# Performance work log

Hardware: AMD Instinct MI355X
Metric: run time of the kernel (lower is better)

## Reference

```python
import jax, jax.numpy as jnp
import numpy as np

NMS_KS = 15
TOP_K = 2048
GAUSS_KS = 7
GAUSS_SIGMA = 1.0
LOSS_LAMBDA = 1.0


def setup_inputs() -> dict:
    key = jax.random.key(0)
    k1, k2, k3 = jax.random.split(key, 3)
    B, H, W = 16, 1024, 1024
    score1 = jax.random.uniform(k1, (B, 1, H, W), dtype=jnp.float32)
    w_score2 = jax.random.uniform(k2, (B, 1, H, W), dtype=jnp.float32)
    w_vis_mask2 = jax.random.randint(k3, (B, 1, H, W), 0, 2) > 0
    return {"score1": score1, "w_score2": w_score2, "w_vis_mask2": w_vis_mask2}


def _nms(score, ks):
    # keep only local maxima within a ks x ks window (stride 1, 'same' padding)
    pooled = jax.lax.reduce_window(score, -jnp.inf, jax.lax.max,
                                   (1, 1, ks, ks), (1, 1, 1, 1), 'SAME')
    return jnp.where(score == pooled, score, jnp.zeros_like(score))


def _prepare_gt_score(score, nms_ks, k, mask):
    # NMS -> mask -> per-image top-k -> binary GT keypoint map
    s = _nms(score, nms_ks) * mask.astype(score.dtype)
    b = s.shape[0]
    flat = s.reshape(b, -1)                      # B x (H*W)
    _, idx = jax.lax.top_k(flat, k)              # B x k
    gt = jnp.zeros_like(flat).at[jnp.arange(b)[:, None], idx].set(1.0)
    return gt.reshape(s.shape)


def _gaussian_filter(x, ks, sigma):
    coords = jnp.arange(ks, dtype=jnp.float32) - (ks - 1) / 2.0
    g = jnp.exp(-(coords ** 2) / (2.0 * sigma ** 2))
    g = g / g.sum()
    k2d = jnp.outer(g, g)[None, None]
    pad = ks // 2
    return jax.lax.conv_general_dilated(
        x, k2d, (1, 1), [(pad, pad), (pad, pad)],
        dimension_numbers=('NCHW', 'OIHW', 'NCHW'))


def reference(score1, w_score2, w_vis_mask2):
    b = score1.shape[0]
    gt_score1 = jax.lax.stop_gradient(
        _prepare_gt_score(w_score2, NMS_KS, TOP_K, w_vis_mask2))
    gt_score1 = _gaussian_filter(gt_score1, GAUSS_KS, GAUSS_SIGMA)
    m = w_vis_mask2.astype(jnp.float32)
    loss = ((score1 - gt_score1) ** 2) * m       # masked elementwise MSE
    loss = loss.reshape(b, -1).sum(-1) / jnp.clip(m.reshape(b, -1).sum(-1), 1e-8)
    return LOSS_LAMBDA * loss.mean()
```

## Files before the change

kernel.cpp:

```cpp
#include <hip/hip_runtime.h>
#include <math.h>

#define BATCH 16
#define H 1024
#define W 1024
#define HR 46
#define CGW 20
#define CGP 21
#define NTILES 8192
#define CAP 4096
#define TOPK 2048
#define BCAP 40

struct WS {
  double term1[BATCH];
  double corr[BATCH];
  unsigned int masksum[BATCH];
  int cand_count[BATCH];
  int   tile_cnt[NTILES];
  float pt1[NTILES * 4];
  int   pmc[NTILES * 4];
  float tile_val[NTILES * BCAP];
  int   tile_idx[NTILES * BCAP];
  float ccand_val[BATCH * CAP];
  int   ccand_idx[BATCH * CAP];
};

__constant__ float GW[7] = {
  0.004433048175f, 0.054005582623f, 0.242036229376f, 0.399050279652f,
  0.242036229376f, 0.054005582623f, 0.004433048175f
};

__device__ __forceinline__ float4 max4(float4 a, float4 b) {
  float4 r;
  r.x = fmaxf(a.x, b.x); r.y = fmaxf(a.y, b.y);
  r.z = fmaxf(a.z, b.z); r.w = fmaxf(a.w, b.w);
  return r;
}

__global__ __launch_bounds__(256, 6) void k_nms(const float* __restrict__ score1,
                                                const float* __restrict__ score2,
                                                const int* __restrict__ mask,
                                                WS* __restrict__ ws) {
  __shared__ float4 halo[HR][CGP];
  __shared__ float4 rmax[32][CGP];
  __shared__ float s_cv[BCAP];
  __shared__ int   s_ci[BCAP];
  __shared__ int   s_cnt;
  const int tid = threadIdx.x;

  const int t = (blockIdx.x & 7) * (NTILES / 8) + (blockIdx.x >> 3);
  const int b  = t >> 9;
  const int tt = t & 511;
  const int ty0 = (tt >> 4) << 5;
  const int tx0 = (tt & 15) << 6;
  const size_t ibase = (size_t)b * ((size_t)H * W);

  if (tid == 0) s_cnt = 0;

  float4 st[4];
  int hr_[4], hc_[4];
  const bool interior = (ty0 >= 7) && (ty0 + 38 < H) && (tx0 >= 8) && (tx0 + 71 < W);
  if (interior) {
    #pragma unroll
    for (int k = 0; k < 4; k++) {
      int i = tid + (k << 8);
      if (i < HR * CGW) {
        int r = i / CGW, c = i - r * CGW;
        hr_[k] = r; hc_[k] = c;
        st[k] = *((const float4*)(score2 + ibase + (size_t)(ty0 - 7 + r) * W + (tx0 - 8)) + c);
      }
    }
  } else {
    #pragma unroll
    for (int k = 0; k < 4; k++) {
      int i = tid + (k << 8);
      if (i < HR * CGW) {
        int r = i / CGW, c = i - r * CGW;
        hr_[k] = r; hc_[k] = c;
        int gy = ty0 - 7 + r, gx = tx0 - 8 + (c << 2);
        float vv[4] = {-INFINITY, -INFINITY, -INFINITY, -INFINITY};
        if (gy >= 0 && gy < H) {
          const float* rp = score2 + ibase + (size_t)gy * W;
          #pragma unroll
          for (int u = 0; u < 4; u++) {
            int gxu = gx + u;
            if (gxu >= 0 && gxu < W) vv[u] = rp[gxu];
          }
        }
        st[k] = make_float4(vv[0], vv[1], vv[2], vv[3]);
      }
    }
  }
  const int prow = tid >> 3;
  const int c8   = tid & 7;
  const size_t pb = ibase + (size_t)(ty0 + prow) * W + tx0 + (c8 << 3);
  const float4 s1a = *(const float4*)(score1 + pb);
  const float4 s1b = *(const float4*)(score1 + pb + 4);
  const int4  mka = *(const int4*)(mask + pb);
  const int4  mkb = *(const int4*)(mask + pb + 4);

  #pragma unroll
  for (int k = 0; k < 4; k++) {
    int i = tid + (k << 8);
    if (i < HR * CGW) halo[hr_[k]][hc_[k]] = st[k];
  }
  __syncthreads();

  if (tid < 160) {
    const int rr = tid / 20;
    const int cg = tid - rr * 20;
    const int R0 = rr << 2;
    float4 core = halo[R0 + 3][cg];
    #pragma unroll
    for (int k = 4; k <= 14; k++) core = max4(core, halo[R0 + k][cg]);
    const float4 h0 = halo[R0][cg], h1 = halo[R0 + 1][cg], h2 = halo[R0 + 2][cg];
    const float4 h15 = halo[R0 + 15][cg], h16 = halo[R0 + 16][cg], h17 = halo[R0 + 17][cg];
    const float4 p2 = h2, p1 = max4(h1, p2), p0 = max4(h0, p1);
    const float4 sf15 = h15, sf16 = max4(sf15, h16), sf17 = max4(sf16, h17);
    rmax[R0 + 0][cg] = max4(core, p0);
    rmax[R0 + 1][cg] = max4(max4(core, p1), sf15);
    rmax[R0 + 2][cg] = max4(max4(core, p2), sf16);
    rmax[R0 + 3][cg] = max4(core, sf17);
  }

  float t1 = 0.f; int mcnt = 0; unsigned int mbits = 0;
  {
    const float sc[8] = {s1a.x, s1a.y, s1a.z, s1a.w, s1b.x, s1b.y, s1b.z, s1b.w};
    const int   mm[8] = {mka.x, mka.y, mka.z, mka.w, mkb.x, mkb.y, mkb.z, mkb.w};
    #pragma unroll
    for (int j = 0; j < 8; j++) {
      if (mm[j]) { t1 = fmaf(sc[j], sc[j], t1); mcnt++; mbits |= (1u << j); }
    }
  }
  __syncthreads();

  float r[24];
  #pragma unroll
  for (int g = 0; g < 6; g++) {
    float4 v = rmax[prow][(c8 << 1) + g];
    r[4 * g + 0] = v.x; r[4 * g + 1] = v.y; r[4 * g + 2] = v.z; r[4 * g + 3] = v.w;
  }
  float core = r[8];
  #pragma unroll
  for (int k = 9; k <= 15; k++) core = fmaxf(core, r[k]);
  const float q7 = r[7];
  const float q6 = fmaxf(r[6], q7);
  const float q5 = fmaxf(r[5], q6);
  const float q4 = fmaxf(r[4], q5);
  const float q3 = fmaxf(r[3], q4);
  const float q2 = fmaxf(r[2], q3);
  const float q1 = fmaxf(r[1], q2);
  float sa[7];
  sa[0] = r[16];
  #pragma unroll
  for (int k = 1; k < 7; k++) sa[k] = fmaxf(sa[k - 1], r[16 + k]);
  float pooled[8];
  pooled[0] = fmaxf(core, q1);
  pooled[1] = fmaxf(fmaxf(core, q2), sa[0]);
  pooled[2] = fmaxf(fmaxf(core, q3), sa[1]);
  pooled[3] = fmaxf(fmaxf(core, q4), sa[2]);
  pooled[4] = fmaxf(fmaxf(core, q5), sa[3]);
  pooled[5] = fmaxf(fmaxf(core, q6), sa[4]);
  pooled[6] = fmaxf(fmaxf(core, q7), sa[5]);
  pooled[7] = fmaxf(core, sa[6]);

  const float4 cva = halo[prow + 7][(c8 << 1) + 2];
  const float4 cvb = halo[prow + 7][(c8 << 1) + 3];
  const float cc[8] = {cva.x, cva.y, cva.z, cva.w, cvb.x, cvb.y, cvb.z, cvb.w};
  #pragma unroll
  for (int j = 0; j < 8; j++) {
    if ((mbits >> j) & 1u) {
      const float s = cc[j];
      if (s == pooled[j] && s > 0.f) {
        int slot = atomicAdd(&s_cnt, 1);
        if (slot < BCAP) {
          s_cv[slot] = s;
          s_ci[slot] = (ty0 + prow) * W + tx0 + (c8 << 3) + j;
        }
      }
    }
  }
  #pragma unroll
  for (int off = 32; off > 0; off >>= 1) {
    t1 += __shfl_down(t1, off);
    mcnt += __shfl_down(mcnt, off);
  }
  if ((tid & 63) == 0) {
    ws->pt1[t * 4 + (tid >> 6)] = t1;
    ws->pmc[t * 4 + (tid >> 6)] = mcnt;
  }
  __syncthreads();
  int cnt = s_cnt; if (cnt > BCAP) cnt = BCAP;
  if (tid == 0) ws->tile_cnt[t] = cnt;
  if (tid < cnt) {
    ws->tile_val[t * BCAP + tid] = s_cv[tid];
    ws->tile_idx[t * BCAP + tid] = s_ci[tid];
  }
}

__global__ __launch_bounds__(256) void k_compact(WS* __restrict__ ws) {
  const int b = blockIdx.x;
  const int tid = threadIdx.x;
  const int lane = tid & 63, w = tid >> 6;
  __shared__ double sF[4];
  __shared__ int    sI[4];
  __shared__ int    wt[4];

  double tsum = 0.0; int msum = 0;
  for (int j = tid; j < 2048; j += 256) {
    tsum += (double)ws->pt1[b * 2048 + j];
    msum += ws->pmc[b * 2048 + j];
  }
  #pragma unroll
  for (int off = 32; off > 0; off >>= 1) {
    tsum += __shfl_down(tsum, off);
    msum += __shfl_down(msum, off);
  }
  if (lane == 0) { sF[w] = tsum; sI[w] = msum; }

  const int tg = b * 512 + 2 * tid;
  int c0 = ws->tile_cnt[tg];     if (c0 > BCAP) c0 = BCAP;
  int c1 = ws->tile_cnt[tg + 1]; if (c1 > BCAP) c1 = BCAP;
  const int pairs = c0 + c1;
  int v = pairs;
  #pragma unroll
  for (int off = 1; off < 64; off <<= 1) {
    int u = __shfl_up(v, off);
    if (lane >= off) v += u;
  }
  if (lane == 63) wt[w] = v;
  __syncthreads();
  if (tid == 0) {
    ws->term1[b] = (sF[0] + sF[1]) + (sF[2] + sF[3]);
    ws->masksum[b] = (unsigned int)(sI[0] + sI[1] + sI[2] + sI[3]);
    ws->corr[b] = 0.0;
  }
  int wo = 0;
  #pragma unroll
  for (int k = 0; k < 4; k++) if (k < w) wo += wt[k];
  const int excl = v - pairs + wo;
  float* dv = ws->ccand_val + b * CAP;
  int*   di = ws->ccand_idx + b * CAP;
  if (tid == 255) {
    int tot = excl + pairs;
    if (tot > CAP) tot = CAP;
    ws->cand_count[b] = tot;
    #pragma unroll
    for (int u = 0; u < 3; u++)
      if (tot + u < CAP) dv[tot + u] = 0.f;
  }
  const float* sv0 = ws->tile_val + (size_t)tg * BCAP;
  const int*   si0 = ws->tile_idx + (size_t)tg * BCAP;
  for (int j = 0; j < c0; j++) {
    int o = excl + j;
    if (o < CAP) { dv[o] = sv0[j]; di[o] = si0[j]; }
  }
  for (int j = 0; j < c1; j++) {
    int o = excl + c0 + j;
    if (o < CAP) { dv[o] = sv0[BCAP + j]; di[o] = si0[BCAP + j]; }
  }
}

__global__ __launch_bounds__(256, 4) void k_rankstamp(const float* __restrict__ score1,
                                                      const int* __restrict__ mask,
                                                      WS* __restrict__ ws) {
  const int blk = (blockIdx.x & 7) * 128 + (blockIdx.x >> 3);
  const int b = blk >> 6;
  const int slice = blk & 63;
  int n = ws->cand_count[b]; if (n > CAP) n = CAP;
  const int i0 = slice << 6;
  if (i0 >= n) return;
  __shared__ __align__(16) float sval[CAP];
  __shared__ __align__(16) int   sidx[CAP];
  __shared__ int   s_prank[4][64];
  __shared__ int   s_keys[64];
  __shared__ int   s_nk;
  __shared__ float cred[4];
  const int tid = threadIdx.x;
  const int nf4 = (n + 3) >> 2;

  const float4* gv = (const float4*)(ws->ccand_val + b * CAP);
  const int4*   gi = (const int4*)(ws->ccand_idx + b * CAP);
  for (int j = tid; j < nf4; j += 256) {
    ((float4*)sval)[j] = gv[j];
    ((int4*)sidx)[j]   = gi[j];
  }
  __syncthreads();

  const int w = tid >> 6, l = tid & 63;
  const float vi = sval[i0 + l];
  const int   xi = sidx[i0 + l];
  const int q = (nf4 + 3) >> 2;
  int lo = w * q; if (lo > nf4) lo = nf4;
  int hi = lo + q; if (hi > nf4) hi = nf4;
  int rank = 0;
  int j = lo;
  for (; j + 4 <= hi; j += 4) {
    #pragma unroll
    for (int u = 0; u < 4; u++) {
      const float4 v = ((const float4*)sval)[j + u];
      const int4  iv = ((const int4*)sidx)[j + u];
      rank += (v.x > vi) + (v.y > vi) + (v.z > vi) + (v.w > vi);
      rank += (v.x == vi && iv.x < xi);
      rank += (v.y == vi && iv.y < xi);
      rank += (v.z == vi && iv.z < xi);
      rank += (v.w == vi && iv.w < xi);
    }
  }
  for (; j < hi; j++) {
    const float4 v = ((const float4*)sval)[j];
    const int4  iv = ((const int4*)sidx)[j];
    rank += (v.x > vi) + (v.y > vi) + (v.z > vi) + (v.w > vi);
    rank += (v.x == vi && iv.x < xi);
    rank += (v.y == vi && iv.y < xi);
    rank += (v.z == vi && iv.z < xi);
    rank += (v.w == vi && iv.w < xi);
  }
  s_prank[w][l] = rank;
  __syncthreads();

  if (tid < 64) {
    const int rtot = s_prank[0][tid] + s_prank[1][tid] + s_prank[2][tid] + s_prank[3][tid];
    const bool sel = (i0 + tid < n) && (rtot < TOPK);
    const unsigned long long bal = __ballot(sel);
    if (sel) {
      const int pos = __popcll(bal & ((1ull << tid) - 1ull));
      s_keys[pos] = sidx[i0 + tid];
    }
    if (tid == 0) s_nk = (int)__popcll(bal);
  }
  __syncthreads();
  const int nk = s_nk;

  float contrib = 0.f;
  const int sub = tid & 7;
  const size_t ib2 = (size_t)b * ((size_t)H * W);
  #pragma unroll
  for (int rnd = 0; rnd < 2; rnd++) {
    const int k = (tid >> 3) + (rnd << 5);
    if (k < nk && sub < 7) {
      const int ck = s_keys[k];
      const int cy = ck >> 10, cx = ck & 1023;
      const int py = cy + sub - 3;
      const float wy = GW[sub] * ((py >= 0 && py < H) ? 1.f : 0.f);
      const int pyc = min(max(py, 0), H - 1);
      const float* s1r = score1 + ib2 + (size_t)pyc * W;
      const int*   mr  = mask   + ib2 + (size_t)pyc * W;
      #pragma unroll
      for (int dx = -3; dx <= 3; dx++) {
        const int px = cx + dx;
        const float wv = wy * GW[dx + 3] * ((px >= 0 && px < W) ? 1.f : 0.f);
        const int pxc = min(max(px, 0), W - 1);
        const float mf = (mr[pxc] != 0) ? 1.f : 0.f;
        contrib += mf * wv * (wv - 2.f * s1r[pxc]);
      }
    }
  }
  #pragma unroll
  for (int off = 32; off > 0; off >>= 1) contrib += __shfl_down(contrib, off);
  if ((tid & 63) == 0) cred[tid >> 6] = contrib;
  __syncthreads();
  if (tid == 0)
    atomicAdd(&ws->corr[b], (double)((cred[0] + cred[1]) + (cred[2] + cred[3])));
}

__global__ void k_final(WS* __restrict__ ws, float* __restrict__ out) {
  const int t = threadIdx.x;
  double v = 0.0;
  if (t < BATCH) {
    double denom = (double)ws->masksum[t];
    if (denom < 1e-8) denom = 1e-8;
    v = (ws->term1[t] + ws->corr[t]) / denom;
  }
  #pragma unroll
  for (int off = 32; off > 0; off >>= 1) v += __shfl_down(v, off);
  if (t == 0) out[0] = (float)(v / BATCH);
}

extern "C" void kernel_launch(void* const* d_in, const int* in_sizes, int n_in,
                              void* d_out, int out_size, void* d_ws, size_t ws_size,
                              hipStream_t stream) {
  const float* score1 = (const float*)d_in[0];
  const float* score2 = (const float*)d_in[1];
  const int*   mask   = (const int*)d_in[2];
  float* out = (float*)d_out;
  WS* ws = (WS*)d_ws;

  k_nms<<<NTILES, 256, 0, stream>>>(score1, score2, mask, ws);
  k_compact<<<BATCH, 256, 0, stream>>>(ws);
  k_rankstamp<<<BATCH * 64, 256, 0, stream>>>(score1, mask, ws);
  k_final<<<1, 64, 0, stream>>>(ws, out);
}
```

Baseline: 82.26 us.

## Make NMS row-max per-wave and emit candidates via wave ballot per band

Each wave now computes the row maxima for its own eight rows, so the second block-wide barrier is replaced by a wave barrier plus an LDS wait. Candidate collection switches from a shared-memory atomic counter plus a final block barrier to a per-wave ballot and popcount, written straight to per-band global slots. Each 8-pixel thread group now keeps at most one local maximum, which holds because the 15x15 window allows at most one maximum per 8 columns. Compaction now scans 8 bands per thread instead of 2 tiles. The rows a wave reads from the halo and from rmax must be written only by that wave, and each band is capped at 12 candidates.

```diff
diff --git a/kernel.cpp b/kernel.cpp
--- a/kernel.cpp
+++ b/kernel.cpp
@@ -8,20 +8,21 @@
 #define CGW 20
 #define CGP 21
 #define NTILES 8192
+#define NBANDS (NTILES * 4)
 #define CAP 4096
 #define TOPK 2048
-#define BCAP 40
+#define BCW 12
 
 struct WS {
   double term1[BATCH];
   double corr[BATCH];
   unsigned int masksum[BATCH];
   int cand_count[BATCH];
-  int   tile_cnt[NTILES];
-  float pt1[NTILES * 4];
-  int   pmc[NTILES * 4];
-  float tile_val[NTILES * BCAP];
-  int   tile_idx[NTILES * BCAP];
+  int   band_cnt[NBANDS];
+  float pt1[NBANDS];
+  int   pmc[NBANDS];
+  float band_val[NBANDS * BCW];
+  int   band_idx[NBANDS * BCW];
   float ccand_val[BATCH * CAP];
   int   ccand_idx[BATCH * CAP];
 };
@@ -44,9 +45,6 @@
                                                 WS* __restrict__ ws) {
   __shared__ float4 halo[HR][CGP];
   __shared__ float4 rmax[32][CGP];
-  __shared__ float s_cv[BCAP];
-  __shared__ int   s_ci[BCAP];
-  __shared__ int   s_cnt;
   const int tid = threadIdx.x;
 
   const int t = (blockIdx.x & 7) * (NTILES / 8) + (blockIdx.x >> 3);
@@ -55,8 +53,6 @@
   const int ty0 = (tt >> 4) << 5;
   const int tx0 = (tt & 15) << 6;
   const size_t ibase = (size_t)b * ((size_t)H * W);
-
-  if (tid == 0) s_cnt = 0;
 
   float4 st[4];
   int hr_[4], hc_[4];
@@ -92,9 +88,11 @@
       }
     }
   }
-  const int prow = tid >> 3;
-  const int c8   = tid & 7;
-  const size_t pb = ibase + (size_t)(ty0 + prow) * W + tx0 + (c8 << 3);
+  const int w  = tid >> 6;
+  const int l  = tid & 63;
+  const int rt = (w << 3) + (l >> 3);
+  const int c8 = l & 7;
+  const size_t pb = ibase + (size_t)(ty0 + rt) * W + tx0 + (c8 << 3);
   const float4 s1a = *(const float4*)(score1 + pb);
   const float4 s1b = *(const float4*)(score1 + pb + 4);
   const int4  mka = *(const int4*)(mask + pb);
@@ -105,12 +103,22 @@
     int i = tid + (k << 8);
     if (i < HR * CGW) halo[hr_[k]][hc_[k]] = st[k];
   }
-  __syncthreads();
-
-  if (tid < 160) {
-    const int rr = tid / 20;
-    const int cg = tid - rr * 20;
-    const int R0 = rr << 2;
+
+  float t1 = 0.f; int mcnt = 0; unsigned int mbits = 0;
+  {
+    const float sc[8] = {s1a.x, s1a.y, s1a.z, s1a.w, s1b.x, s1b.y, s1b.z, s1b.w};
+    const int   mm[8] = {mka.x, mka.y, mka.z, mka.w, mkb.x, mkb.y, mkb.z, mkb.w};
+    #pragma unroll
+    for (int j = 0; j < 8; j++) {
+      if (mm[j]) { t1 = fmaf(sc[j], sc[j], t1); mcnt++; mbits |= (1u << j); }
+    }
+  }
+  __syncthreads();
+
+  if (l < 40) {
+    const int r2 = l / 20;
+    const int cg = l - r2 * 20;
+    const int R0 = (w << 3) + (r2 << 2);
     float4 core = halo[R0 + 3][cg];
     #pragma unroll
     for (int k = 4; k <= 14; k++) core = max4(core, halo[R0 + k][cg]);
@@ -123,22 +131,14 @@
     rmax[R0 + 2][cg] = max4(max4(core, p2), sf16);
     rmax[R0 + 3][cg] = max4(core, sf17);
   }
-
-  float t1 = 0.f; int mcnt = 0; unsigned int mbits = 0;
-  {
-    const float sc[8] = {s1a.x, s1a.y, s1a.z, s1a.w, s1b.x, s1b.y, s1b.z, s1b.w};
-    const int   mm[8] = {mka.x, mka.y, mka.z, mka.w, mkb.x, mkb.y, mkb.z, mkb.w};
-    #pragma unroll
-    for (int j = 0; j < 8; j++) {
-      if (mm[j]) { t1 = fmaf(sc[j], sc[j], t1); mcnt++; mbits |= (1u << j); }
-    }
-  }
-  __syncthreads();
+  __builtin_amdgcn_wave_barrier();
+  asm volatile("s_waitcnt lgkmcnt(0)" ::: "memory");
+  __builtin_amdgcn_sched_barrier(0);
 
   float r[24];
   #pragma unroll
   for (int g = 0; g < 6; g++) {
-    float4 v = rmax[prow][(c8 << 1) + g];
+    float4 v = rmax[rt][(c8 << 1) + g];
     r[4 * g + 0] = v.x; r[4 * g + 1] = v.y; r[4 * g + 2] = v.z; r[4 * g + 3] = v.w;
   }
   float core = r[8];
@@ -165,20 +165,24 @@
   pooled[6] = fmaxf(fmaxf(core, q7), sa[5]);
   pooled[7] = fmaxf(core, sa[6]);
 
-  const float4 cva = halo[prow + 7][(c8 << 1) + 2];
-  const float4 cvb = halo[prow + 7][(c8 << 1) + 3];
+  const float4 cva = halo[rt + 7][(c8 << 1) + 2];
+  const float4 cvb = halo[rt + 7][(c8 << 1) + 3];
   const float cc[8] = {cva.x, cva.y, cva.z, cva.w, cvb.x, cvb.y, cvb.z, cvb.w};
+  int   cj = -1; float cv = 0.f;
   #pragma unroll
   for (int j = 0; j < 8; j++) {
-    if ((mbits >> j) & 1u) {
+    if (((mbits >> j) & 1u) && cj < 0) {
       const float s = cc[j];
-      if (s == pooled[j] && s > 0.f) {
-        int slot = atomicAdd(&s_cnt, 1);
-        if (slot < BCAP) {
-          s_cv[slot] = s;
-          s_ci[slot] = (ty0 + prow) * W + tx0 + (c8 << 3) + j;
-        }
-      }
+      if (s == pooled[j] && s > 0.f) { cj = j; cv = s; }
+    }
+  }
+  const int band = (t << 2) + w;
+  const unsigned long long bal = __ballot(cj >= 0);
+  if (cj >= 0) {
+    const int pos = (int)__popcll(bal & ((1ull << l) - 1ull));
+    if (pos < BCW) {
+      ws->band_val[band * BCW + pos] = cv;
+      ws->band_idx[band * BCW + pos] = (ty0 + rt) * W + tx0 + (c8 << 3) + cj;
     }
   }
   #pragma unroll
@@ -186,16 +190,11 @@
     t1 += __shfl_down(t1, off);
     mcnt += __shfl_down(mcnt, off);
   }
-  if ((tid & 63) == 0) {
-    ws->pt1[t * 4 + (tid >> 6)] = t1;
-    ws->pmc[t * 4 + (tid >> 6)] = mcnt;
-  }
-  __syncthreads();
-  int cnt = s_cnt; if (cnt > BCAP) cnt = BCAP;
-  if (tid == 0) ws->tile_cnt[t] = cnt;
-  if (tid < cnt) {
-    ws->tile_val[t * BCAP + tid] = s_cv[tid];
-    ws->tile_idx[t * BCAP + tid] = s_ci[tid];
+  if (l == 0) {
+    int nc = (int)__popcll(bal); if (nc > BCW) nc = BCW;
+    ws->band_cnt[band] = nc;
+    ws->pt1[band] = t1;
+    ws->pmc[band] = mcnt;
   }
 }
 
@@ -219,11 +218,15 @@
   }
   if (lane == 0) { sF[w] = tsum; sI[w] = msum; }
 
-  const int tg = b * 512 + 2 * tid;
-  int c0 = ws->tile_cnt[tg];     if (c0 > BCAP) c0 = BCAP;
-  int c1 = ws->tile_cnt[tg + 1]; if (c1 > BCAP) c1 = BCAP;
-  const int pairs = c0 + c1;
-  int v = pairs;
+  const int base = b * 2048 + tid * 8;
+  int c[8]; int csum = 0;
+  #pragma unroll
+  for (int u = 0; u < 8; u++) {
+    int x = ws->band_cnt[base + u];
+    if (x > BCW) x = BCW;
+    c[u] = x; csum += x;
+  }
+  int v = csum;
   #pragma unroll
   for (int off = 1; off < 64; off <<= 1) {
     int u = __shfl_up(v, off);
@@ -239,26 +242,26 @@
   int wo = 0;
   #pragma unroll
   for (int k = 0; k < 4; k++) if (k < w) wo += wt[k];
-  const int excl = v - pairs + wo;
+  const int excl = v - csum + wo;
   float* dv = ws->ccand_val + b * CAP;
   int*   di = ws->ccand_idx + b * CAP;
   if (tid == 255) {
-    int tot = excl + pairs;
+    int tot = excl + csum;
     if (tot > CAP) tot = CAP;
     ws->cand_count[b] = tot;
     #pragma unroll
     for (int u = 0; u < 3; u++)
       if (tot + u < CAP) dv[tot + u] = 0.f;
   }
-  const float* sv0 = ws->tile_val + (size_t)tg * BCAP;
-  const int*   si0 = ws->tile_idx + (size_t)tg * BCAP;
-  for (int j = 0; j < c0; j++) {
-    int o = excl + j;
-    if (o < CAP) { dv[o] = sv0[j]; di[o] = si0[j]; }
-  }
-  for (int j = 0; j < c1; j++) {
-    int o = excl + c0 + j;
-    if (o < CAP) { dv[o] = sv0[BCAP + j]; di[o] = si0[BCAP + j]; }
+  int off = excl;
+  #pragma unroll
+  for (int u = 0; u < 8; u++) {
+    const float* sv = ws->band_val + (size_t)(base + u) * BCW;
+    const int*   si = ws->band_idx + (size_t)(base + u) * BCW;
+    for (int j = 0; j < c[u]; j++) {
+      if (off < CAP) { dv[off] = sv[j]; di[off] = si[j]; }
+      off++;
+    }
   }
 }
 
```

Result: slower. 85.82 us (+4.3%).
